# Optimization experiments

Hardware: AMD Instinct MI355X
Metric: run time of the kernel (lower is better)

The kernel has to match this reference:

```python
import jax, jax.numpy as jnp
import numpy as np

V, C, H, T, B, D = 32000, 768, 12, 1024, 2, 4
HID = C // 2
FF = 4 * C
HD = C // H


def _ln(x, s, b):
    m = jnp.mean(x, axis=-1, keepdims=True)
    v = jnp.mean((x - m) ** 2, axis=-1, keepdims=True)
    return (x - m) * jax.lax.rsqrt(v + 1e-5) * s + b


def setup_inputs() -> dict:
    key = jax.random.key(0)
    ks = jax.random.split(key, 12)
    nrm = lambda k, shp: 0.02 * jax.random.normal(k, shp, dtype=jnp.float32)
    return {
        "idx": jax.random.randint(ks[0], (B, T), 0, V),
        "tok_emb": nrm(ks[1], (V, C)),
        "pos_emb": nrm(ks[2], (T, C)),
        "r_w1": nrm(ks[3], (C, HID)), "r_b1": jnp.zeros((HID,), jnp.float32),
        "r_w2": nrm(ks[4], (HID, D)), "r_b2": jnp.zeros((D,), jnp.float32),
        "ln1_s": jnp.ones((C,), jnp.float32), "ln1_b": jnp.zeros((C,), jnp.float32),
        "qkv_w": nrm(ks[5], (C, 3 * C)),
        "proj_w": nrm(ks[6], (C, C)), "proj_b": jnp.zeros((C,), jnp.float32),
        "ln2_s": jnp.ones((C,), jnp.float32), "ln2_b": jnp.zeros((C,), jnp.float32),
        "f_w1": nrm(ks[7], (C, FF)), "f_b1": jnp.zeros((FF,), jnp.float32),
        "f_w2": nrm(ks[8], (FF, C)), "f_b2": jnp.zeros((C,), jnp.float32),
        "lnf_s": jnp.ones((C,), jnp.float32), "lnf_b": jnp.zeros((C,), jnp.float32),
        "head_w": nrm(ks[9], (V, C)),  # torch Linear weight [out, in]
    }


def reference(idx, tok_emb, pos_emb, r_w1, r_b1, r_w2, r_b2,
              ln1_s, ln1_b, qkv_w, proj_w, proj_b, ln2_s, ln2_b,
              f_w1, f_b1, f_w2, f_b2, lnf_s, lnf_b, head_w):
    # embeddings
    x = tok_emb[idx] + pos_emb[None, :, :]  # [B,T,C]

    # depth router (eval mode: hard one-hot argmax, k=1)
    rh = jax.nn.relu(x @ r_w1 + r_b1)
    r_logits = rh @ r_w2 + r_b2  # [B,T,D]
    w = jax.nn.one_hot(jnp.argmax(r_logits, axis=-1), D, dtype=x.dtype)  # [B,T,D]

    causal = jnp.tril(jnp.ones((T, T), dtype=bool))
    scale = 1.0 / np.sqrt(HD).astype(np.float32)

    def block(z):
        # pre-norm attention
        y = _ln(z, ln1_s, ln1_b)
        qkv = y @ qkv_w  # [B,T,3C]
        q, k, v = jnp.split(qkv, 3, axis=-1)
        q = q.reshape(B, T, H, HD)
        k = k.reshape(B, T, H, HD)
        v = v.reshape(B, T, H, HD)
        att = jnp.einsum('bqhd,bkhd->bhqk', q, k) * scale
        att = jnp.where(causal, att, -jnp.inf)
        att = jax.nn.softmax(att, axis=-1)
        o = jnp.einsum('bhqk,bkhd->bqhd', att, v).reshape(B, T, C)
        z = z + (o @ proj_w + proj_b)
        # pre-norm FFN (dropout inactive in eval)
        y2 = _ln(z, ln2_s, ln2_b)
        ff = jax.nn.gelu(y2 @ f_w1 + f_b1, approximate=False) @ f_w2 + f_b2
        return z + ff

    # depth-d output = block applied (d+1) times; accumulate with router weight
    out = jnp.zeros_like(x)
    h = x
    for d in range(D):
        h = block(h)
        out = out + w[:, :, d:d + 1] * h

    xf = _ln(out, lnf_s, lnf_b)
    logits = xf @ head_w.T  # [B,T,V]
    return logits
```

## Files before the change

kernel.cpp:

```cpp
#include <hip/hip_runtime.h>
#include <hip/hip_bf16.h>

typedef unsigned short u16;
typedef __bf16 bf16x8 __attribute__((ext_vector_type(8)));
typedef float f32x4 __attribute__((ext_vector_type(4)));

#define DEVINL __device__ __forceinline__

DEVINL u16 f2b(float f){
  unsigned u = __float_as_uint(f);
  u += 0x7FFFu + ((u >> 16) & 1u);
  return (u16)(u >> 16);
}
DEVINL float b2f(u16 b){ return __uint_as_float(((unsigned)b) << 16); }

DEVINL void gload16(const void* g, void* l){
  __builtin_amdgcn_global_load_lds(
      (const __attribute__((address_space(1))) unsigned*)g,
      (__attribute__((address_space(3))) unsigned*)l, 16, 0, 0);
}

__global__ __launch_bounds__(256) void k_embed(const int* __restrict__ idx,
    const float* __restrict__ tok, const float* __restrict__ pos, float* __restrict__ h){
  int r = blockIdx.x, t = threadIdx.x;
  int token = idx[r];
  const float* tr = tok + (long)token * 768;
  const float* pr = pos + (long)(r & 1023) * 768;
  float* hr = h + (long)r * 768;
  hr[t]       = tr[t]       + pr[t];
  hr[t + 256] = tr[t + 256] + pr[t + 256];
  hr[t + 512] = tr[t + 512] + pr[t + 512];
}

__global__ __launch_bounds__(256) void k_ln(const float* __restrict__ X,
    const float* __restrict__ s, const float* __restrict__ b, u16* __restrict__ Y){
  int r = blockIdx.x, t = threadIdx.x;
  const float* x = X + (long)r * 768;
  float v0 = x[t], v1 = x[t + 256], v2 = x[t + 512];
  float sum = v0 + v1 + v2;
  __shared__ float tmp[4];
  #pragma unroll
  for (int o = 32; o; o >>= 1) sum += __shfl_xor(sum, o);
  int wave = t >> 6;
  if ((t & 63) == 0) tmp[wave] = sum;
  __syncthreads();
  sum = tmp[0] + tmp[1] + tmp[2] + tmp[3];
  float m = sum * (1.f / 768.f);
  float d0 = v0 - m, d1 = v1 - m, d2 = v2 - m;
  float sq = d0 * d0 + d1 * d1 + d2 * d2;
  #pragma unroll
  for (int o = 32; o; o >>= 1) sq += __shfl_xor(sq, o);
  __syncthreads();
  if ((t & 63) == 0) tmp[wave] = sq;
  __syncthreads();
  sq = tmp[0] + tmp[1] + tmp[2] + tmp[3];
  float rs = rsqrtf(sq * (1.f / 768.f) + 1e-5f);
  u16* y = Y + (long)r * 768;
  y[t]       = f2b(d0 * rs * s[t]       + b[t]);
  y[t + 256] = f2b(d1 * rs * s[t + 256] + b[t + 256]);
  y[t + 512] = f2b(d2 * rs * s[t + 512] + b[t + 512]);
}

__global__ __launch_bounds__(256) void k_wt(const float* __restrict__ W, u16* __restrict__ Wt,
                                            int K, int N){
  __shared__ float tile[32][33];
  int kb = blockIdx.x * 32, nb = blockIdx.y * 32;
  int tx = threadIdx.x & 31, ty = threadIdx.x >> 5;
  #pragma unroll
  for (int i = 0; i < 32; i += 8) tile[ty + i][tx] = W[(long)(kb + ty + i) * N + nb + tx];
  __syncthreads();
  #pragma unroll
  for (int i = 0; i < 32; i += 8) Wt[(long)(nb + ty + i) * K + kb + tx] = f2b(tile[tx][ty + i]);
}

__global__ __launch_bounds__(256) void k_conv(const float* __restrict__ W, u16* __restrict__ O, long n4){
  long i = (long)blockIdx.x * 256 + threadIdx.x;
  if (i >= n4) return;
  float4 v = ((const float4*)W)[i];
  unsigned lo = (unsigned)f2b(v.x) | ((unsigned)f2b(v.y) << 16);
  unsigned hi = (unsigned)f2b(v.z) | ((unsigned)f2b(v.w) << 16);
  ((uint2*)O)[i] = make_uint2(lo, hi);
}

__global__ __launch_bounds__(256) void k_r1(const float* __restrict__ A, const float* __restrict__ B,
    const float* __restrict__ bias, float* __restrict__ C){
  __shared__ float As[64][17];
  __shared__ float Bs[16][65];
  int r0 = blockIdx.x * 64, c0 = blockIdx.y * 64;
  int t = threadIdx.x;
  int tx = t & 15, ty = t >> 4;
  float acc[4][4] = {};
  for (int k0 = 0; k0 < 768; k0 += 16){
    #pragma unroll
    for (int i = 0; i < 4; i++){ int e = i * 256 + t; As[e >> 4][e & 15] = A[(long)(r0 + (e >> 4)) * 768 + k0 + (e & 15)]; }
    #pragma unroll
    for (int i = 0; i < 4; i++){ int e = i * 256 + t; Bs[e >> 6][e & 63] = B[(long)(k0 + (e >> 6)) * 384 + c0 + (e & 63)]; }
    __syncthreads();
    #pragma unroll
    for (int kk = 0; kk < 16; kk++){
      float a[4], bb[4];
      #pragma unroll
      for (int i = 0; i < 4; i++) a[i] = As[ty * 4 + i][kk];
      #pragma unroll
      for (int j = 0; j < 4; j++) bb[j] = Bs[kk][tx * 4 + j];
      #pragma unroll
      for (int i = 0; i < 4; i++)
        #pragma unroll
        for (int j = 0; j < 4; j++) acc[i][j] += a[i] * bb[j];
    }
    __syncthreads();
  }
  #pragma unroll
  for (int i = 0; i < 4; i++)
    #pragma unroll
    for (int j = 0; j < 4; j++){
      int rr = r0 + ty * 4 + i, cc = c0 + tx * 4 + j;
      float v = acc[i][j] + bias[cc];
      C[(long)rr * 384 + cc] = v > 0.f ? v : 0.f;
    }
}

__global__ __launch_bounds__(64) void k_r2(const float* __restrict__ rh, const float* __restrict__ w2,
    const float* __restrict__ b2, int* __restrict__ sel){
  int tkn = blockIdx.x, l = threadIdx.x;
  float s0 = 0, s1 = 0, s2 = 0, s3 = 0;
  const float* r = rh + (long)tkn * 384;
  for (int k = l; k < 384; k += 64){
    float rv = r[k];
    float4 w = ((const float4*)w2)[k];
    s0 += rv * w.x; s1 += rv * w.y; s2 += rv * w.z; s3 += rv * w.w;
  }
  #pragma unroll
  for (int o = 32; o; o >>= 1){
    s0 += __shfl_xor(s0, o); s1 += __shfl_xor(s1, o);
    s2 += __shfl_xor(s2, o); s3 += __shfl_xor(s3, o);
  }
  if (l == 0){
    float v[4] = { s0 + b2[0], s1 + b2[1], s2 + b2[2], s3 + b2[3] };
    int am = 0; float bv = v[0];
    #pragma unroll
    for (int j = 1; j < 4; j++) if (v[j] > bv){ bv = v[j]; am = j; }
    sel[tkn] = am;
  }
}

__global__ __launch_bounds__(256) void k_softmax(u16* S){
  int q = blockIdx.x, z = blockIdx.y;
  u16* row = S + (long)z * 1048576 + (long)q * 1024;
  int t = threadIdx.x;
  uint2 raw = make_uint2(0u, 0u);
  if (t * 4 <= q) raw = ((const uint2*)row)[t];
  float vals[4];
  vals[0] = b2f((u16)(raw.x & 0xFFFF));
  vals[1] = b2f((u16)(raw.x >> 16));
  vals[2] = b2f((u16)(raw.y & 0xFFFF));
  vals[3] = b2f((u16)(raw.y >> 16));
  #pragma unroll
  for (int j = 0; j < 4; j++){
    int c = t * 4 + j;
    vals[j] = (c <= q) ? vals[j] * 0.125f : -1e30f;
  }
  float m = fmaxf(fmaxf(vals[0], vals[1]), fmaxf(vals[2], vals[3]));
  __shared__ float tmp[4], tmp2[4];
  #pragma unroll
  for (int o = 32; o; o >>= 1) m = fmaxf(m, __shfl_xor(m, o));
  int wave = t >> 6;
  if ((t & 63) == 0) tmp[wave] = m;
  __syncthreads();
  m = fmaxf(fmaxf(tmp[0], tmp[1]), fmaxf(tmp[2], tmp[3]));
  float e[4]; float sum = 0.f;
  #pragma unroll
  for (int j = 0; j < 4; j++){
    int c = t * 4 + j;
    e[j] = (c <= q) ? expf(vals[j] - m) : 0.f;
    sum += e[j];
  }
  #pragma unroll
  for (int o = 32; o; o >>= 1) sum += __shfl_xor(sum, o);
  if ((t & 63) == 0) tmp2[wave] = sum;
  __syncthreads();
  sum = tmp2[0] + tmp2[1] + tmp2[2] + tmp2[3];
  float inv = 1.f / sum;
  unsigned w0 = (unsigned)f2b(e[0] * inv) | ((unsigned)f2b(e[1] * inv) << 16);
  unsigned w1 = (unsigned)f2b(e[2] * inv) | ((unsigned)f2b(e[3] * inv) << 16);
  ((uint2*)row)[t] = make_uint2(w0, w1);
}

__global__ __launch_bounds__(256) void k_redln(const float* __restrict__ P, int nparts,
    const float* __restrict__ bias, const float* __restrict__ resid, float* __restrict__ outh,
    const float* __restrict__ ls, const float* __restrict__ lb, u16* __restrict__ Y,
    const int* __restrict__ sel, float* __restrict__ outb, int d){
  int r = blockIdx.x, t = threadIdx.x;
  float v0, v1, v2;
  {
    float a0 = bias[t]       + resid[(long)r * 768 + t];
    float a1 = bias[t + 256] + resid[(long)r * 768 + t + 256];
    float a2 = bias[t + 512] + resid[(long)r * 768 + t + 512];
    for (int p = 0; p < nparts; p++){
      const float* pr = P + ((long)p * 2048 + r) * 768;
      a0 += pr[t]; a1 += pr[t + 256]; a2 += pr[t + 512];
    }
    v0 = a0; v1 = a1; v2 = a2;
  }
  float* hr = outh + (long)r * 768;
  hr[t] = v0; hr[t + 256] = v1; hr[t + 512] = v2;
  if (sel && sel[r] == d){
    float* orow = outb + (long)r * 768;
    orow[t] = v0; orow[t + 256] = v1; orow[t + 512] = v2;
  }
  float sum = v0 + v1 + v2;
  __shared__ float tmp[4];
  #pragma unroll
  for (int o = 32; o; o >>= 1) sum += __shfl_xor(sum, o);
  int wave = t >> 6;
  if ((t & 63) == 0) tmp[wave] = sum;
  __syncthreads();
  sum = tmp[0] + tmp[1] + tmp[2] + tmp[3];
  float m = sum * (1.f / 768.f);
  float d0 = v0 - m, d1 = v1 - m, d2 = v2 - m;
  float sq = d0 * d0 + d1 * d1 + d2 * d2;
  #pragma unroll
  for (int o = 32; o; o >>= 1) sq += __shfl_xor(sq, o);
  __syncthreads();
  if ((t & 63) == 0) tmp[wave] = sq;
  __syncthreads();
  sq = tmp[0] + tmp[1] + tmp[2] + tmp[3];
  float rs = rsqrtf(sq * (1.f / 768.f) + 1e-5f);
  u16* y = Y + (long)r * 768;
  y[t]       = f2b(d0 * rs * ls[t]       + lb[t]);
  y[t + 256] = f2b(d1 * rs * ls[t + 256] + lb[t + 256]);
  y[t + 512] = f2b(d2 * rs * ls[t + 512] + lb[t + 512]);
}

__global__ __launch_bounds__(64) void k_gemm1(
    const u16* __restrict__ A, int lda, long s1A, long s2A,
    const u16* __restrict__ B, int ldb, long s1B, long s2B,
    void* Cv, int ldc, long s1C, long s2C,
    const float* __restrict__ bias,
    const float* __restrict__ resid, int ldr,
    int K, int zdiv, int ksegK, int flags, u16* __restrict__ vtbuf){
  __shared__ __align__(16) u16 As[2][64][32];
  __shared__ __align__(16) u16 Bs[2][64][32];
  int lane = threadIdx.x;
  int bx = blockIdx.x, by = blockIdx.y, bz = blockIdx.z;
  if (flags & 16){
    int nx = gridDim.x, nwg = nx * gridDim.y;
    int lin = by * nx + bx;
    int q = nwg >> 3;
    int nl = (lin & 7) * q + (lin >> 3);
    bx = nl % nx; by = nl / nx;
  }
  if (flags & 4){
    int i = 0, x = bx;
    while (((i + 1) * (i + 2)) >> 1 <= x) i++;
    bx = i; by = x - ((i * (i + 1)) >> 1);
  }
  int row0 = bx * 64, col0 = by * 64;
  int zq = bz / zdiv, zr = bz % zdiv;
  A += zq * s2A + (long)zr * s1A;
  B += zq * s2B + (long)zr * s1B;
  long coff = zq * s2C + (long)zr * s1C;
  int kstart = 0, Klim = K;
  if (ksegK > 0){ kstart = bz * ksegK; Klim = kstart + ksegK; }
  else if (flags & 8) Klim = min(K, row0 + 64);
  f32x4 acc[4][4] = {};
  int lr = lane & 15, lk = (lane >> 4) * 8;
  int srow = lane >> 2, scol = (lane & 3) * 16;
  int nt = (Klim - kstart) >> 5;
  auto STAGE = [&](int buf, int k0){
    #pragma unroll
    for (int i = 0; i < 4; i++)
      gload16((const char*)&A[(long)(row0 + i * 16 + srow) * lda + k0] + scol, &As[buf][i * 16][0]);
    #pragma unroll
    for (int i = 0; i < 4; i++)
      gload16((const char*)&B[(long)(col0 + i * 16 + srow) * ldb + k0] + scol, &Bs[buf][i * 16][0]);
  };
  STAGE(0, kstart);
  int cur = 0;
  for (int t = 0; t < nt; t++){
    if (t + 1 < nt){
      STAGE(cur ^ 1, kstart + ((t + 1) << 5));
      asm volatile("s_waitcnt vmcnt(8)" ::: "memory");
    } else {
      asm volatile("s_waitcnt vmcnt(0)" ::: "memory");
    }
    __builtin_amdgcn_sched_barrier(0);
    bf16x8 af[4], bb[4];
    #pragma unroll
    for (int i = 0; i < 4; i++)
      af[i] = __builtin_bit_cast(bf16x8, *(const uint4*)&As[cur][i * 16 + lr][lk]);
    #pragma unroll
    for (int j = 0; j < 4; j++)
      bb[j] = __builtin_bit_cast(bf16x8, *(const uint4*)&Bs[cur][j * 16 + lr][lk]);
    #pragma unroll
    for (int i = 0; i < 4; i++)
      #pragma unroll
      for (int j = 0; j < 4; j++)
        acc[i][j] = __builtin_amdgcn_mfma_f32_16x16x32_bf16(af[i], bb[j], acc[i][j], 0, 0, 0);
    __builtin_amdgcn_sched_barrier(0);
    cur ^= 1;
  }
  bool vmode = (vtbuf != nullptr) && (col0 >= 1536);
  if (vmode){
    #pragma unroll
    for (int i = 0; i < 4; i++){
      int rbase = row0 + i * 16 + ((lane >> 4) << 2);
      int b = rbase >> 10, tt = rbase & 1023;
      #pragma unroll
      for (int j = 0; j < 4; j++){
        int cc = col0 + j * 16 + lr;
        int hh = (cc - 1536) >> 6, dd = (cc - 1536) & 63;
        unsigned lo = (unsigned)f2b(acc[i][j][0]) | ((unsigned)f2b(acc[i][j][1]) << 16);
        unsigned hi = (unsigned)f2b(acc[i][j][2]) | ((unsigned)f2b(acc[i][j][3]) << 16);
        *(uint2*)&vtbuf[((long)(b * 12 + hh) * 64 + dd) * 1024 + tt] = make_uint2(lo, hi);
      }
    }
    return;
  }
  #pragma unroll
  for (int i = 0; i < 4; i++){
    int rbase = row0 + i * 16 + ((lane >> 4) << 2);
    #pragma unroll
    for (int j = 0; j < 4; j++){
      int cc = col0 + j * 16 + lr;
      #pragma unroll
      for (int q = 0; q < 4; q++){
        int rr = rbase + q;
        float v = acc[i][j][q];
        if (bias) v += bias[cc];
        if (flags & 2) v = 0.5f * v * (1.f + erff(v * 0.70710678118654752f));
        if (resid) v += resid[(long)rr * ldr + cc];
        if (flags & 1) ((u16*)Cv)[coff + (long)rr * ldc + cc] = f2b(v);
        else           ((float*)Cv)[coff + (long)rr * ldc + cc] = v;
      }
    }
  }
}

template<int BM, int BN>
__global__ __launch_bounds__(256) void k_gemm(
    const u16* __restrict__ A, int lda,
    const u16* __restrict__ B, int ldb,
    void* Cv, int ldc,
    int K, int flags){
  constexpr int FM = BM / 32, FN = BN / 32;
  __shared__ __align__(16) u16 As[BM][32];
  __shared__ __align__(16) u16 Bs[BN][32];
  int t = threadIdx.x;
  int wave = t >> 6, lane = t & 63;
  int wm = wave >> 1, wn = wave & 1;
  int bx = blockIdx.x, by = blockIdx.y;
  if (flags & 16){
    int nx = gridDim.x, nwg = nx * gridDim.y;
    int lin = by * nx + bx;
    int q = nwg >> 3;
    int nl = (lin & 7) * q + (lin >> 3);
    bx = nl % nx; by = nl / nx;
  }
  int row0 = bx * BM, col0 = by * BN;
  f32x4 acc[FM][FN] = {};
  int lr = lane & 15, lk = (lane >> 4) * 8;
  int lrow = lane >> 2, lcolb = (lane & 3) * 16;
  for (int k0 = 0; k0 < K; k0 += 32){
    #pragma unroll
    for (int i = 0; i < BM / 64; i++){
      int r = i * 64 + wave * 16;
      gload16((const char*)&A[(long)(row0 + r + lrow) * lda + k0] + lcolb, &As[r][0]);
    }
    #pragma unroll
    for (int i = 0; i < BN / 64; i++){
      int r = i * 64 + wave * 16;
      gload16((const char*)&B[(long)(col0 + r + lrow) * ldb + k0] + lcolb, &Bs[r][0]);
    }
    __syncthreads();
    bf16x8 af[FM], bfr[FN];
    #pragma unroll
    for (int i = 0; i < FM; i++)
      af[i] = __builtin_bit_cast(bf16x8, *(const uint4*)&As[wm * FM * 16 + i * 16 + lr][lk]);
    #pragma unroll
    for (int j = 0; j < FN; j++)
      bfr[j] = __builtin_bit_cast(bf16x8, *(const uint4*)&Bs[wn * FN * 16 + j * 16 + lr][lk]);
    #pragma unroll
    for (int i = 0; i < FM; i++)
      #pragma unroll
      for (int j = 0; j < FN; j++)
        acc[i][j] = __builtin_amdgcn_mfma_f32_16x16x32_bf16(af[i], bfr[j], acc[i][j], 0, 0, 0);
    __syncthreads();
  }
  #pragma unroll
  for (int i = 0; i < FM; i++){
    int rbase = row0 + wm * FM * 16 + i * 16 + (lane >> 4) * 4;
    #pragma unroll
    for (int j = 0; j < FN; j++){
      int cc = col0 + wn * FN * 16 + j * 16 + lr;
      #pragma unroll
      for (int q = 0; q < 4; q++){
        int rr = rbase + q;
        ((float*)Cv)[(long)rr * ldc + cc] = acc[i][j][q];
      }
    }
  }
}

extern "C" void kernel_launch(void* const* d_in, const int* in_sizes, int n_in,
                              void* d_out, int out_size, void* d_ws, size_t ws_size,
                              hipStream_t stream){
  const int*   idx    = (const int*)d_in[0];
  const float* tok    = (const float*)d_in[1];
  const float* pos    = (const float*)d_in[2];
  const float* r_w1   = (const float*)d_in[3];
  const float* r_b1   = (const float*)d_in[4];
  const float* r_w2   = (const float*)d_in[5];
  const float* r_b2   = (const float*)d_in[6];
  const float* ln1_s  = (const float*)d_in[7];
  const float* ln1_b  = (const float*)d_in[8];
  const float* qkv_w  = (const float*)d_in[9];
  const float* proj_w = (const float*)d_in[10];
  const float* proj_b = (const float*)d_in[11];
  const float* ln2_s  = (const float*)d_in[12];
  const float* ln2_b  = (const float*)d_in[13];
  const float* f_w1   = (const float*)d_in[14];
  const float* f_b1   = (const float*)d_in[15];
  const float* f_w2   = (const float*)d_in[16];
  const float* f_b2   = (const float*)d_in[17];
  const float* lnf_s  = (const float*)d_in[18];
  const float* lnf_b  = (const float*)d_in[19];
  const float* head_w = (const float*)d_in[20];
  float* logits = (float*)d_out;

  char* w = (char*)d_ws;
  size_t off = 0;
  auto alloc = [&](size_t bytes)->char*{ char* p = w + off; off += (bytes + 255) & ~(size_t)255; return p; };
  u16*   wqT  = (u16*)  alloc(2304ull * 768 * 2);
  u16*   wpT  = (u16*)  alloc(768ull * 768 * 2);
  u16*   wf1T = (u16*)  alloc(3072ull * 768 * 2);
  u16*   wf2T = (u16*)  alloc(768ull * 3072 * 2);
  u16*   whd  = (u16*)  alloc(32000ull * 768 * 2);
  float* h    = (float*)alloc(2048ull * 768 * 4);
  float* outb = (float*)alloc(2048ull * 768 * 4);
  u16*   y    = (u16*)  alloc(2048ull * 768 * 2);
  u16*   qkv  = (u16*)  alloc(2048ull * 2304 * 2);
  u16*   o    = (u16*)  alloc(2048ull * 768 * 2);
  u16*   ffh  = (u16*)  alloc(2048ull * 3072 * 2);
  u16*   Vt   = (u16*)  alloc(24ull * 64 * 1024 * 2);
  float* rh   = (float*)alloc(2048ull * 384 * 4);
  int*   sel  = (int*)  alloc(2048 * 4);
  size_t fixed = off;
  size_t sBig = 24ull * 1024 * 1024 * 2;
  size_t sPart = 4ull * 2048 * 768 * 4;
  bool bigS = (ws_size >= fixed + (sBig > sPart ? sBig : sPart) + 4096);
  char* Sraw = alloc(bigS ? (sBig > sPart ? sBig : sPart)
                          : (12ull * 1024 * 1024 * 2 > sPart ? 12ull * 1024 * 1024 * 2 : sPart));
  u16*   S  = (u16*)Sraw;
  float* Sf = (float*)Sraw;
  (void)in_sizes; (void)n_in; (void)out_size;

  dim3 b256(256), b64(64);
  k_wt<<<dim3(24, 72), b256, 0, stream>>>(qkv_w,  wqT,  768, 2304);
  k_wt<<<dim3(24, 24), b256, 0, stream>>>(proj_w, wpT,  768, 768);
  k_wt<<<dim3(24, 96), b256, 0, stream>>>(f_w1,   wf1T, 768, 3072);
  k_wt<<<dim3(96, 24), b256, 0, stream>>>(f_w2,   wf2T, 3072, 768);
  k_conv<<<24000, b256, 0, stream>>>(head_w, whd, 6144000);
  k_embed<<<2048, b256, 0, stream>>>(idx, tok, pos, h);
  k_r1<<<dim3(32, 6), b256, 0, stream>>>(h, r_w1, r_b1, rh);
  k_r2<<<2048, b64, 0, stream>>>(rh, r_w2, r_b2, sel);
  k_ln<<<2048, b256, 0, stream>>>(h, ln1_s, ln1_b, y);

  for (int d = 0; d < 4; ++d){
    k_gemm1<<<dim3(32, 36), b64, 0, stream>>>(
        y, 768, 0, 0, wqT, 768, 0, 0, qkv, 2304, 0, 0,
        nullptr, nullptr, 0, 768, 12, 0, 1 | 16, Vt);
    if (bigS){
      k_gemm1<<<dim3(136, 1, 24), b64, 0, stream>>>(
          qkv, 2304, 64, 1024ll * 2304, qkv + 768, 2304, 64, 1024ll * 2304,
          S, 1024, 1048576, 12ll * 1048576, nullptr, nullptr, 0, 64, 12, 0, 1 | 4 | 16, nullptr);
      k_softmax<<<dim3(1024, 24), b256, 0, stream>>>(S);
      k_gemm1<<<dim3(16, 1, 24), b64, 0, stream>>>(
          S, 1024, 1048576, 12ll * 1048576, Vt, 1024, 65536, 12ll * 65536,
          o, 768, 64, 786432, nullptr, nullptr, 0, 1024, 12, 0, 1 | 8 | 16, nullptr);
    } else {
      for (int b = 0; b < 2; b++){
        const u16* Qp = qkv + (long)b * 1024 * 2304;
        k_gemm1<<<dim3(136, 1, 12), b64, 0, stream>>>(
            Qp, 2304, 64, 0, Qp + 768, 2304, 64, 0,
            S, 1024, 1048576, 0, nullptr, nullptr, 0, 64, 12, 0, 1 | 4 | 16, nullptr);
        k_softmax<<<dim3(1024, 12), b256, 0, stream>>>(S);
        k_gemm1<<<dim3(16, 1, 12), b64, 0, stream>>>(
            S, 1024, 1048576, 0, Vt + (long)b * 786432, 1024, 65536, 0,
            o + (long)b * 786432, 768, 64, 0, nullptr, nullptr, 0, 1024, 12, 0, 1 | 8 | 16, nullptr);
      }
    }
    k_gemm1<<<dim3(32, 12, 4), b64, 0, stream>>>(
        o, 768, 0, 0, wpT, 768, 0, 0, Sf, 768, 2048ll * 768, 0,
        nullptr, nullptr, 0, 768, 12, 192, 16, nullptr);
    k_redln<<<2048, b256, 0, stream>>>(Sf, 4, proj_b, h, h, ln2_s, ln2_b, y,
                                       nullptr, nullptr, 0);
    k_gemm1<<<dim3(32, 48), b64, 0, stream>>>(
        y, 768, 0, 0, wf1T, 768, 0, 0, ffh, 3072, 0, 0,
        f_b1, nullptr, 0, 768, 12, 0, 1 | 2 | 16, nullptr);
    k_gemm1<<<dim3(32, 12, 4), b64, 0, stream>>>(
        ffh, 3072, 0, 0, wf2T, 3072, 0, 0, Sf, 768, 2048ll * 768, 0,
        nullptr, nullptr, 0, 3072, 12, 768, 16, nullptr);
    k_redln<<<2048, b256, 0, stream>>>(Sf, 4, f_b2, h, h, ln1_s, ln1_b, y,
                                       sel, outb, d);
  }
  k_ln<<<2048, b256, 0, stream>>>(outb, lnf_s, lnf_b, y);
  k_gemm<128, 128><<<dim3(16, 250), b256, 0, stream>>>(
      y, 768, whd, 768, logits, 32000, 768, 16);
}
```

Measured before the change: 1.088 ms.

## Replace QK/softmax/PV three-kernel attention with fused flash-attention kernel

Replaces the per-depth attention path (QK^T GEMM writing a full bf16 score matrix, a separate softmax pass, then a PV GEMM) with a single fused kernel that keeps scores in registers and uses an online softmax over causal 64-wide KV tiles. This is meant to remove the global-memory round trips of the 24x1024x1024 score buffer and two kernel launches per depth. The trade-off is a grid of only 16x24 workgroups with uneven causal work per tile and a serial KV loop per block, which may underuse the GPU.

```diff
diff --git a/kernel.cpp b/kernel.cpp
--- a/kernel.cpp
+++ b/kernel.cpp
@@ -144,46 +144,110 @@
   }
 }
 
-__global__ __launch_bounds__(256) void k_softmax(u16* S){
-  int q = blockIdx.x, z = blockIdx.y;
-  u16* row = S + (long)z * 1048576 + (long)q * 1024;
-  int t = threadIdx.x;
-  uint2 raw = make_uint2(0u, 0u);
-  if (t * 4 <= q) raw = ((const uint2*)row)[t];
-  float vals[4];
-  vals[0] = b2f((u16)(raw.x & 0xFFFF));
-  vals[1] = b2f((u16)(raw.x >> 16));
-  vals[2] = b2f((u16)(raw.y & 0xFFFF));
-  vals[3] = b2f((u16)(raw.y >> 16));
+__global__ __launch_bounds__(256) void k_attn(
+    const u16* __restrict__ qkv, const u16* __restrict__ Vt, u16* __restrict__ o){
+  __shared__ __align__(16) u16 Klds[64][64];
+  __shared__ __align__(16) u16 Vlds[64][64];
+  __shared__ __align__(16) u16 Plds[4][16][72];
+  int qt = blockIdx.x, bh = blockIdx.y;
+  int b = bh / 12, hh = bh % 12;
+  int t = threadIdx.x, w = t >> 6, lane = t & 63;
+  int lr = lane & 15, koct = lane >> 4;
+  int q0 = qt * 64 + w * 16;
+  const u16* Qrow = qkv + ((long)(b * 1024 + q0 + lr)) * 2304 + hh * 64;
+  bf16x8 qf[2];
+  qf[0] = __builtin_bit_cast(bf16x8, *(const uint4*)&Qrow[koct * 8]);
+  qf[1] = __builtin_bit_cast(bf16x8, *(const uint4*)&Qrow[32 + koct * 8]);
+  f32x4 oacc[4] = {};
+  float m_run[4], l_run[4];
+  #pragma unroll
+  for (int r = 0; r < 4; r++){ m_run[r] = -1e30f; l_run[r] = 0.f; }
+  int srow8 = lane >> 3, scolb = (lane & 7) * 16;
+  const char* Kbase = (const char*)(qkv + (long)b * 1024 * 2304 + 768 + hh * 64);
+  const char* Vbase = (const char*)(Vt + (long)bh * 64 * 1024);
+  for (int kvt = 0; kvt <= qt; ++kvt){
+    #pragma unroll
+    for (int i = 0; i < 2; i++){
+      int row = w * 16 + i * 8 + srow8;
+      int sb = scolb ^ ((row & 7) << 4);
+      gload16(Kbase + (long)(kvt * 64 + row) * 4608 + sb, &Klds[w * 16 + i * 8][0]);
+    }
+    #pragma unroll
+    for (int i = 0; i < 2; i++){
+      int row = w * 16 + i * 8 + srow8;
+      int sb = scolb ^ ((row & 7) << 4);
+      gload16(Vbase + (long)row * 2048 + kvt * 128 + sb, &Vlds[w * 16 + i * 8][0]);
+    }
+    __syncthreads();
+    f32x4 sacc[4] = {};
+    #pragma unroll
+    for (int j = 0; j < 4; j++){
+      #pragma unroll
+      for (int f = 0; f < 2; f++){
+        int row = 16 * j + lr;
+        bf16x8 kf = __builtin_bit_cast(bf16x8, *(const uint4*)(
+            (const char*)&Klds[0][0] + row * 128 + ((64 * f + koct * 16) ^ ((row & 7) << 4))));
+        sacc[j] = __builtin_amdgcn_mfma_f32_16x16x32_bf16(qf[f], kf, sacc[j], 0, 0, 0);
+      }
+    }
+    bool diag = (kvt == qt);
+    float p[4][4];
+    #pragma unroll
+    for (int r = 0; r < 4; r++){
+      int qg = q0 + 4 * koct + r;
+      float vj[4];
+      #pragma unroll
+      for (int j = 0; j < 4; j++){
+        int kvg = kvt * 64 + 16 * j + lr;
+        float v = sacc[j][r] * 0.125f;
+        vj[j] = (!diag || kvg <= qg) ? v : -1e30f;
+      }
+      float mx = fmaxf(fmaxf(vj[0], vj[1]), fmaxf(vj[2], vj[3]));
+      #pragma unroll
+      for (int s = 1; s < 16; s <<= 1) mx = fmaxf(mx, __shfl_xor(mx, s));
+      float mn = fmaxf(m_run[r], mx);
+      float sc = __expf(m_run[r] - mn);
+      float rs = 0.f;
+      #pragma unroll
+      for (int j = 0; j < 4; j++){ p[j][r] = __expf(vj[j] - mn); rs += p[j][r]; }
+      #pragma unroll
+      for (int s = 1; s < 16; s <<= 1) rs += __shfl_xor(rs, s);
+      l_run[r] = l_run[r] * sc + rs;
+      m_run[r] = mn;
+      #pragma unroll
+      for (int j = 0; j < 4; j++) oacc[j][r] *= sc;
+    }
+    #pragma unroll
+    for (int r = 0; r < 4; r++)
+      #pragma unroll
+      for (int j = 0; j < 4; j++)
+        Plds[w][4 * koct + r][16 * j + lr] = f2b(p[j][r]);
+    bf16x8 pf[2];
+    pf[0] = __builtin_bit_cast(bf16x8, *(const uint4*)&Plds[w][lr][koct * 8]);
+    pf[1] = __builtin_bit_cast(bf16x8, *(const uint4*)&Plds[w][lr][32 + koct * 8]);
+    #pragma unroll
+    for (int j = 0; j < 4; j++){
+      #pragma unroll
+      for (int f = 0; f < 2; f++){
+        int row = 16 * j + lr;
+        bf16x8 vf = __builtin_bit_cast(bf16x8, *(const uint4*)(
+            (const char*)&Vlds[0][0] + row * 128 + ((64 * f + koct * 16) ^ ((row & 7) << 4))));
+        oacc[j] = __builtin_amdgcn_mfma_f32_16x16x32_bf16(pf[f], vf, oacc[j], 0, 0, 0);
+      }
+    }
+    __syncthreads();
+  }
+  float inv[4];
+  #pragma unroll
+  for (int r = 0; r < 4; r++) inv[r] = 1.f / l_run[r];
   #pragma unroll
   for (int j = 0; j < 4; j++){
-    int c = t * 4 + j;
-    vals[j] = (c <= q) ? vals[j] * 0.125f : -1e30f;
-  }
-  float m = fmaxf(fmaxf(vals[0], vals[1]), fmaxf(vals[2], vals[3]));
-  __shared__ float tmp[4], tmp2[4];
-  #pragma unroll
-  for (int o = 32; o; o >>= 1) m = fmaxf(m, __shfl_xor(m, o));
-  int wave = t >> 6;
-  if ((t & 63) == 0) tmp[wave] = m;
-  __syncthreads();
-  m = fmaxf(fmaxf(tmp[0], tmp[1]), fmaxf(tmp[2], tmp[3]));
-  float e[4]; float sum = 0.f;
-  #pragma unroll
-  for (int j = 0; j < 4; j++){
-    int c = t * 4 + j;
-    e[j] = (c <= q) ? expf(vals[j] - m) : 0.f;
-    sum += e[j];
-  }
-  #pragma unroll
-  for (int o = 32; o; o >>= 1) sum += __shfl_xor(sum, o);
-  if ((t & 63) == 0) tmp2[wave] = sum;
-  __syncthreads();
-  sum = tmp2[0] + tmp2[1] + tmp2[2] + tmp2[3];
-  float inv = 1.f / sum;
-  unsigned w0 = (unsigned)f2b(e[0] * inv) | ((unsigned)f2b(e[1] * inv) << 16);
-  unsigned w1 = (unsigned)f2b(e[2] * inv) | ((unsigned)f2b(e[3] * inv) << 16);
-  ((uint2*)row)[t] = make_uint2(w0, w1);
+    #pragma unroll
+    for (int r = 0; r < 4; r++){
+      int tq = b * 1024 + q0 + 4 * koct + r;
+      o[(long)tq * 768 + hh * 64 + 16 * j + lr] = f2b(oacc[j][r] * inv[r]);
+    }
+  }
 }
 
 __global__ __launch_bounds__(256) void k_redln(const float* __restrict__ P, int nparts,
@@ -250,11 +314,6 @@
     int nl = (lin & 7) * q + (lin >> 3);
     bx = nl % nx; by = nl / nx;
   }
-  if (flags & 4){
-    int i = 0, x = bx;
-    while (((i + 1) * (i + 2)) >> 1 <= x) i++;
-    bx = i; by = x - ((i * (i + 1)) >> 1);
-  }
   int row0 = bx * 64, col0 = by * 64;
   int zq = bz / zdiv, zr = bz % zdiv;
   A += zq * s2A + (long)zr * s1A;
@@ -262,7 +321,6 @@
   long coff = zq * s2C + (long)zr * s1C;
   int kstart = 0, Klim = K;
   if (ksegK > 0){ kstart = bz * ksegK; Klim = kstart + ksegK; }
-  else if (flags & 8) Klim = min(K, row0 + 64);
   f32x4 acc[4][4] = {};
   int lr = lane & 15, lk = (lane >> 4) * 8;
   int srow = lane >> 2, scol = (lane & 3) * 16;
@@ -445,15 +503,8 @@
   u16*   Vt   = (u16*)  alloc(24ull * 64 * 1024 * 2);
   float* rh   = (float*)alloc(2048ull * 384 * 4);
   int*   sel  = (int*)  alloc(2048 * 4);
-  size_t fixed = off;
-  size_t sBig = 24ull * 1024 * 1024 * 2;
-  size_t sPart = 4ull * 2048 * 768 * 4;
-  bool bigS = (ws_size >= fixed + (sBig > sPart ? sBig : sPart) + 4096);
-  char* Sraw = alloc(bigS ? (sBig > sPart ? sBig : sPart)
-                          : (12ull * 1024 * 1024 * 2 > sPart ? 12ull * 1024 * 1024 * 2 : sPart));
-  u16*   S  = (u16*)Sraw;
-  float* Sf = (float*)Sraw;
-  (void)in_sizes; (void)n_in; (void)out_size;
+  float* Sf   = (float*)alloc(4ull * 2048 * 768 * 4);
+  (void)in_sizes; (void)n_in; (void)out_size; (void)ws_size;
 
   dim3 b256(256), b64(64);
   k_wt<<<dim3(24, 72), b256, 0, stream>>>(qkv_w,  wqT,  768, 2304);
@@ -470,26 +521,7 @@
     k_gemm1<<<dim3(32, 36), b64, 0, stream>>>(
         y, 768, 0, 0, wqT, 768, 0, 0, qkv, 2304, 0, 0,
         nullptr, nullptr, 0, 768, 12, 0, 1 | 16, Vt);
-    if (bigS){
-      k_gemm1<<<dim3(136, 1, 24), b64, 0, stream>>>(
-          qkv, 2304, 64, 1024ll * 2304, qkv + 768, 2304, 64, 1024ll * 2304,
-          S, 1024, 1048576, 12ll * 1048576, nullptr, nullptr, 0, 64, 12, 0, 1 | 4 | 16, nullptr);
-      k_softmax<<<dim3(1024, 24), b256, 0, stream>>>(S);
-      k_gemm1<<<dim3(16, 1, 24), b64, 0, stream>>>(
-          S, 1024, 1048576, 12ll * 1048576, Vt, 1024, 65536, 12ll * 65536,
-          o, 768, 64, 786432, nullptr, nullptr, 0, 1024, 12, 0, 1 | 8 | 16, nullptr);
-    } else {
-      for (int b = 0; b < 2; b++){
-        const u16* Qp = qkv + (long)b * 1024 * 2304;
-        k_gemm1<<<dim3(136, 1, 12), b64, 0, stream>>>(
-            Qp, 2304, 64, 0, Qp + 768, 2304, 64, 0,
-            S, 1024, 1048576, 0, nullptr, nullptr, 0, 64, 12, 0, 1 | 4 | 16, nullptr);
-        k_softmax<<<dim3(1024, 12), b256, 0, stream>>>(S);
-        k_gemm1<<<dim3(16, 1, 12), b64, 0, stream>>>(
-            S, 1024, 1048576, 0, Vt + (long)b * 786432, 1024, 65536, 0,
-            o + (long)b * 786432, 768, 64, 0, nullptr, nullptr, 0, 1024, 12, 0, 1 | 8 | 16, nullptr);
-      }
-    }
+    k_attn<<<dim3(16, 24), b256, 0, stream>>>(qkv, Vt, o);
     k_gemm1<<<dim3(32, 12, 4), b64, 0, stream>>>(
         o, 768, 0, 0, wpT, 768, 0, 0, Sf, 768, 2048ll * 768, 0,
         nullptr, nullptr, 0, 768, 12, 192, 16, nullptr);
```

After: 935.0 us. 14.0% less time.
